# Kernel optimization log

Hardware: AMD Instinct MI355X
Metric: run time of the kernel (lower is better)

Reference implementation:

```python
import jax, jax.numpy as jnp
import numpy as np

B, T, D = 1, 2048, 2048
H, HKV, DH = 32, 8, 64          # head_dim = D // H, n_rep = H // HKV
NREP = H // HKV
WINDOW = 1024
NMETA = 128
EPS = 1e-6
ROPE_BASE = 10000.0


def _rmsnorm(x, w):
    # per-head-dim RMSNorm computed in float32 (matches torch module)
    xf = x.astype(jnp.float32)
    rms = jax.lax.rsqrt(jnp.mean(xf * xf, axis=-1, keepdims=True) + EPS)
    return (w * xf * rms).astype(x.dtype)


def _rope(x, pos):
    # x: [B, h, L, DH], pos: [B, L]; interleaved even/odd rotation
    inv_freq = 1.0 / (ROPE_BASE ** (jnp.arange(0, DH, 2, dtype=jnp.float32) / DH))
    freqs = pos.astype(jnp.float32)[..., None] * inv_freq        # [B, L, DH/2]
    cos = jnp.cos(freqs)[:, None]                                # [B, 1, L, DH/2]
    sin = jnp.sin(freqs)[:, None]
    x1, x2 = x[..., ::2], x[..., 1::2]
    rot = jnp.stack([x1 * cos - x2 * sin, x1 * sin + x2 * cos], axis=-1)
    return rot.reshape(x.shape)


def setup_inputs() -> dict:
    key = jax.random.key(0)
    ks = jax.random.split(key, 5)
    s = 0.02
    return {
        "hidden_states": jax.random.normal(ks[0], (B, T, D), jnp.float32),
        "position_ids": jnp.arange(T, dtype=jnp.int32),
        "Wq": jax.random.normal(ks[1], (H * DH, D), jnp.float32) * s,
        "Wk": jax.random.normal(ks[2], (HKV * DH, D), jnp.float32) * s,
        "Wv": jax.random.normal(ks[3], (HKV * DH, D), jnp.float32) * s,
        "Wo": jax.random.normal(ks[4], (D, H * DH), jnp.float32) * s,
        "q_norm_w": jnp.ones((DH,), jnp.float32),
        "k_norm_w": jnp.ones((DH,), jnp.float32),
    }


def reference(hidden_states, position_ids, Wq, Wk, Wv, Wo, q_norm_w, k_norm_w):
    Bn, Tn, _ = hidden_states.shape
    # projections (nn.Linear: x @ W.T)
    q = (hidden_states @ Wq.T).reshape(Bn, Tn, H, DH).transpose(0, 2, 1, 3)   # [B,H,T,DH]
    k = (hidden_states @ Wk.T).reshape(Bn, Tn, HKV, DH).transpose(0, 2, 1, 3)  # [B,HKV,T,DH]
    v = (hidden_states @ Wv.T).reshape(Bn, Tn, HKV, DH).transpose(0, 2, 1, 3)
    q = _rmsnorm(q, q_norm_w)
    k = _rmsnorm(k, k_norm_w)

    Tk = k.shape[2]  # no kv_cache -> Tk == T
    pos_q = position_ids if position_ids.ndim == 2 else jnp.broadcast_to(position_ids[None], (Bn, Tn))
    pos_k = jnp.broadcast_to(jnp.arange(Tk, dtype=jnp.int32)[None], (Bn, Tk))
    q = _rope(q, pos_q[:, -Tn:])
    k = _rope(k, pos_k)

    # GQA repeat_kv
    k = jnp.broadcast_to(k[:, :, None], (Bn, HKV, NREP, Tk, DH)).reshape(Bn, H, Tk, DH)
    v = jnp.broadcast_to(v[:, :, None], (Bn, HKV, NREP, Tk, DH)).reshape(Bn, H, Tk, DH)

    scores = jnp.einsum('bhqd,bhkd->bhqk', q, k) * (DH ** -0.5)

    # sliding-window + meta-token mask (matches _make_swa_mask)
    q_idx = jnp.arange(Tn)[:, None]
    k_idx = jnp.arange(Tk)[None, :]
    offset = Tk - Tn
    abs_q = q_idx + offset
    win_start = jnp.maximum(abs_q - WINDOW + 1, NMETA)
    allowed = ((k_idx >= win_start) & (k_idx <= abs_q)) | (k_idx < NMETA)
    scores = jnp.where(allowed[None, None], scores, -jnp.inf)

    probs = jax.nn.softmax(scores, axis=-1)
    out = jnp.einsum('bhqk,bhkd->bhqd', probs, v)
    out = out.transpose(0, 2, 1, 3).reshape(Bn, Tn, H * DH)
    return out @ Wo.T
```

## Files before the change

### kernel.cpp

```cpp
#include <hip/hip_runtime.h>
#include <hip/hip_bf16.h>
#include <cstdint>

#define TSEQ 2048
#define DMODEL 2048
#define NHEAD 32
#define NKV 8
#define DHEAD 64
#define QKVN 3072
#define AON 2048

using bf16x8 = __attribute__((ext_vector_type(8))) short;
using bf16x4 = __attribute__((ext_vector_type(4))) short;
using f32x4  = __attribute__((ext_vector_type(4))) float;

__device__ __forceinline__ ushort f2bf(float f) {
  union { float f; uint32_t u; } v; v.f = f;
  uint32_t u = v.u;
  return (ushort)((u + 0x7fffu + ((u >> 16) & 1u)) >> 16);
}

__device__ __forceinline__ float fexp2(float x) {
#if __has_builtin(__builtin_amdgcn_exp2f)
  return __builtin_amdgcn_exp2f(x);
#else
  return __expf(x * 0.69314718055994531f);
#endif
}

__device__ __forceinline__ uint32_t cvtpk(float lo, float hi) {
  uint32_t r;
  asm("v_cvt_pk_bf16_f32 %0, %1, %2" : "=v"(r) : "v"(lo), "v"(hi));
  return r;
}

__device__ __forceinline__ void gload16(const void* g, void* l) {
  __builtin_amdgcn_global_load_lds((const __attribute__((address_space(1))) void*)g,
                                   (__attribute__((address_space(3))) void*)l,
                                   16, 0, 0);
}

#define RG0 1048576
#define RG1 2097152
#define RG2 2359296
#define RG3 2621440
__global__ void k_cvt_all(const float* __restrict__ X, const float* __restrict__ Wq,
                          const float* __restrict__ Wk, const float* __restrict__ Wv,
                          const int* __restrict__ pos,
                          ushort* __restrict__ Xb, ushort* __restrict__ Wqkvb,
                          float4* __restrict__ Tbl) {
  int gid = blockIdx.x * blockDim.x + threadIdx.x;
  if (gid < TSEQ * 32) {
    int t = gid >> 5, jj = gid & 31;
    float invf = fexp2((float)jj * (-0.41524101186092029f));
    float qs, qc, ks, kc;
    __sincosf((float)pos[t] * invf, &qs, &qc);
    __sincosf((float)t * invf, &ks, &kc);
    Tbl[gid] = make_float4(qc * 0.18033688011112043f, qs * 0.18033688011112043f, kc, ks);
  }
  int stride = gridDim.x * blockDim.x;
  for (int i = gid; i < RG3; i += stride) {
    const float4* s; ushort4* d;
    if (i < RG0)      { s = (const float4*)X  + i;         d = (ushort4*)Xb + i; }
    else if (i < RG1) { s = (const float4*)Wq + (i - RG0); d = (ushort4*)Wqkvb + (i - RG0); }
    else if (i < RG2) { s = (const float4*)Wk + (i - RG1); d = (ushort4*)Wqkvb + 1048576 + (i - RG1); }
    else              { s = (const float4*)Wv + (i - RG2); d = (ushort4*)Wqkvb + 1310720 + (i - RG2); }
    float4 v = *s;
    ushort4 o;
    o.x = f2bf(v.x); o.y = f2bf(v.y); o.z = f2bf(v.z); o.w = f2bf(v.w);
    *d = o;
  }
}

__global__ __launch_bounds__(512) void k_gemm_qkv(
    const ushort* __restrict__ A, const ushort* __restrict__ B,
    const float* __restrict__ qw, const float* __restrict__ kw,
    const float4* __restrict__ Tbl,
    ushort* __restrict__ Qb, ushort* __restrict__ Kb, ushort* __restrict__ Vt,
    int M, int N, int K)
{
  __shared__ ushort As[4][128 * 32];
  __shared__ ushort Bs[4][128 * 32];
  const int m0 = blockIdx.y * 128, n0 = blockIdx.x * 128;
  const int tid = threadIdx.x;
  const int w = tid >> 6, lane = tid & 63, lg = lane >> 4, lr = lane & 15;
  const int wr = (w >> 1) * 32, wc = (w & 1) * 64;

  f32x4 acc[2][4];
#pragma unroll
  for (int i = 0; i < 2; ++i)
#pragma unroll
    for (int j = 0; j < 4; ++j) acc[i][j] = (f32x4){0.f, 0.f, 0.f, 0.f};

  const int nt = K >> 5;

  auto stage = [&](int b, int t) {
    const int k0 = t << 5;
    {
      int ci = tid;
      int row = ci >> 2, c = ci & 3;
      int clog = c ^ ((row >> 1) & 3);
      gload16(A + (size_t)(m0 + row) * K + k0 + clog * 8, As[b] + ci * 8);
    }
    {
      int ci = tid;
      int row = ci >> 2, c = ci & 3;
      int clog = c ^ ((row >> 1) & 3);
      gload16(B + (size_t)(n0 + row) * K + k0 + clog * 8, Bs[b] + ci * 8);
    }
  };

  stage(0, 0); stage(1, 1); stage(2, 2);

  for (int t = 0; t < nt; ++t) {
    int rem = nt - t;
    if (rem >= 3)      asm volatile("s_waitcnt vmcnt(4)" ::: "memory");
    else if (rem == 2) asm volatile("s_waitcnt vmcnt(2)" ::: "memory");
    else               asm volatile("s_waitcnt vmcnt(0)" ::: "memory");
    __builtin_amdgcn_s_barrier();
    __builtin_amdgcn_sched_barrier(0);

    const ushort* as = As[t & 3];
    const ushort* bs = Bs[t & 3];
    bf16x8 af[2], bfr[4];
#pragma unroll
    for (int i = 0; i < 2; ++i) {
      int ra = wr + i * 16 + lr;
      af[i] = *reinterpret_cast<const bf16x8*>(as + ra * 32 + ((lg ^ ((ra >> 1) & 3)) << 3));
    }
#pragma unroll
    for (int j = 0; j < 4; ++j) {
      int rb = wc + j * 16 + lr;
      bfr[j] = *reinterpret_cast<const bf16x8*>(bs + rb * 32 + ((lg ^ ((rb >> 1) & 3)) << 3));
    }
    asm volatile("s_waitcnt lgkmcnt(0)" ::: "memory");
    __builtin_amdgcn_sched_barrier(0);

    if (t + 3 < nt) stage((t + 3) & 3, t + 3);

#pragma unroll
    for (int i = 0; i < 2; ++i)
#pragma unroll
      for (int j = 0; j < 4; ++j)
        acc[i][j] = __builtin_amdgcn_mfma_f32_16x16x32_bf16(af[i], bfr[j], acc[i][j], 0, 0, 0);
  }

  const int colunit = (n0 + wc) >> 6;
  if (colunit < 40) {
    const bool isQ = (colunit < 32);
    const float* wn = isQ ? qw : kw;
    float wv[4];
#pragma unroll
    for (int j = 0; j < 4; ++j) wv[j] = wn[j * 16 + lr];
    ushort* dst = isQ ? (Qb + (size_t)colunit * TSEQ * 64)
                      : (Kb + (size_t)(colunit - 32) * TSEQ * 64);
#pragma unroll
    for (int i = 0; i < 2; ++i)
#pragma unroll
      for (int r = 0; r < 4; ++r) {
        int row = m0 + wr + i * 16 + lg * 4 + r;
        float ss = 0.f;
#pragma unroll
        for (int j = 0; j < 4; ++j) { float x = acc[i][j][r]; ss += x * x; }
        ss += __shfl_xor(ss, 1); ss += __shfl_xor(ss, 2);
        ss += __shfl_xor(ss, 4); ss += __shfl_xor(ss, 8);
        float rms = rsqrtf(ss * (1.0f / 64.0f) + 1e-6f);
#pragma unroll
        for (int j = 0; j < 4; ++j) {
          float xh = acc[i][j][r] * rms * wv[j];
          float other = __shfl_xor(xh, 1);
          float4 tb = Tbl[(size_t)row * 32 + j * 8 + (lr >> 1)];
          float c = isQ ? tb.x : tb.z;
          float s = isQ ? tb.y : tb.w;
          float outv = (lr & 1) ? (other * s + xh * c) : (xh * c - other * s);
          dst[(size_t)row * 64 + j * 16 + lr] = f2bf(outv);
        }
      }
  } else {
    const int hv = colunit - 40;
#pragma unroll
    for (int i = 0; i < 2; ++i)
#pragma unroll
      for (int j = 0; j < 4; ++j)
#pragma unroll
        for (int r = 0; r < 4; ++r) {
          int row = m0 + wr + i * 16 + lg * 4 + r;
          Vt[((size_t)hv * 64 + j * 16 + lr) * TSEQ + row] = f2bf(acc[i][j][r]);
        }
  }
}

__global__ __launch_bounds__(256) void k_gemm64(
    const ushort* __restrict__ A, const ushort* __restrict__ B,
    float* __restrict__ C, int M, int N, int K)
{
  __shared__ ushort As[4][64 * 32];
  __shared__ ushort Bs[4][128 * 32];
  const int m0 = blockIdx.y * 64, n0 = blockIdx.x * 128;
  const int tid = threadIdx.x;
  const int w = tid >> 6, lane = tid & 63, lg = lane >> 4, lr = lane & 15;
  const int wr = (w >> 1) * 32, wc = (w & 1) * 64;

  f32x4 acc[2][4];
#pragma unroll
  for (int i = 0; i < 2; ++i)
#pragma unroll
    for (int j = 0; j < 4; ++j) acc[i][j] = (f32x4){0.f, 0.f, 0.f, 0.f};

  const int nt = K >> 5;

  auto stage = [&](int b, int t) {
    const int k0 = t << 5;
    {
      int ci = tid;
      int row = ci >> 2, c = ci & 3;
      int clog = c ^ ((row >> 1) & 3);
      gload16(A + (size_t)(m0 + row) * K + k0 + clog * 8, As[b] + ci * 8);
    }
#pragma unroll
    for (int j = 0; j < 2; ++j) {
      int ci = j * 256 + tid;
      int row = ci >> 2, c = ci & 3;
      int clog = c ^ ((row >> 1) & 3);
      gload16(B + (size_t)(n0 + row) * K + k0 + clog * 8, Bs[b] + ci * 8);
    }
  };

  stage(0, 0); stage(1, 1); stage(2, 2);

  for (int t = 0; t < nt; ++t) {
    int rem = nt - t;
    if (rem >= 3)      asm volatile("s_waitcnt vmcnt(6)" ::: "memory");
    else if (rem == 2) asm volatile("s_waitcnt vmcnt(3)" ::: "memory");
    else               asm volatile("s_waitcnt vmcnt(0)" ::: "memory");
    __builtin_amdgcn_s_barrier();
    __builtin_amdgcn_sched_barrier(0);

    const ushort* as = As[t & 3];
    const ushort* bs = Bs[t & 3];
    bf16x8 af[2], bfr[4];
#pragma unroll
    for (int i = 0; i < 2; ++i) {
      int ra = wr + i * 16 + lr;
      af[i] = *reinterpret_cast<const bf16x8*>(as + ra * 32 + ((lg ^ ((ra >> 1) & 3)) << 3));
    }
#pragma unroll
    for (int j = 0; j < 4; ++j) {
      int rb = wc + j * 16 + lr;
      bfr[j] = *reinterpret_cast<const bf16x8*>(bs + rb * 32 + ((lg ^ ((rb >> 1) & 3)) << 3));
    }
    asm volatile("s_waitcnt lgkmcnt(0)" ::: "memory");
    __builtin_amdgcn_sched_barrier(0);

    if (t + 3 < nt) stage((t + 3) & 3, t + 3);

#pragma unroll
    for (int i = 0; i < 2; ++i)
#pragma unroll
      for (int j = 0; j < 4; ++j)
        acc[i][j] = __builtin_amdgcn_mfma_f32_16x16x32_bf16(af[i], bfr[j], acc[i][j], 0, 0, 0);
  }

#pragma unroll
  for (int i = 0; i < 2; ++i)
#pragma unroll
    for (int j = 0; j < 4; ++j)
#pragma unroll
      for (int r = 0; r < 4; ++r)
        C[(size_t)(m0 + wr + i * 16 + lg * 4 + r) * N + n0 + wc + j * 16 + lr] = acc[i][j][r];
}

__global__ __launch_bounds__(512) void k_attn(
    const ushort* __restrict__ Qb, const ushort* __restrict__ Kb,
    const ushort* __restrict__ Vt, ushort* __restrict__ AO,
    const float* __restrict__ Wo, ushort* __restrict__ Wob)
{
  __shared__ ushort Ks[2][64 * 64];
  __shared__ ushort Vs[2][64 * 64];

  const int h = blockIdx.x;
  const int q0 = ((int)gridDim.y - 1 - (int)blockIdx.y) * 128;
  const int tid = threadIdx.x;
  const int w = tid >> 6, lane = tid & 63;
  const int lg = lane >> 4, lr = lane & 15;
  const int qrow = q0 + w * 16 + lr;

  const ushort* qp = Qb + ((size_t)h * TSEQ + qrow) * 64;
  const bf16x8 qf0 = *reinterpret_cast<const bf16x8*>(qp + lg * 8);
  const bf16x8 qf1 = *reinterpret_cast<const bf16x8*>(qp + 32 + lg * 8);
  const int hk = h >> 2;
  const char* Kh = (const char*)(Kb + (size_t)hk * TSEQ * 64);
  const char* Vh = (const char*)(Vt + (size_t)hk * 64 * TSEQ);

  float m = -1e30f, lsum = 0.0f;
  f32x4 o[4];
#pragma unroll
  for (int dt = 0; dt < 4; ++dt) o[dt] = (f32x4){0.f, 0.f, 0.f, 0.f};

  const int wlo = (q0 >= 1152) ? (q0 - 1024) : 128;
  int nwin = (q0 + 64 - wlo) / 64 + 1;
  if (nwin < 0) nwin = 0;
  const int ntiles = 2 + nwin;
  const int qw0 = q0 + w * 16;
  const int wmaxstart = ((qw0 + 15 - 1023) > 128) ? (qw0 + 15 - 1023) : 128;
  const int wminstart = ((qw0 - 1023) > 128) ? (qw0 - 1023) : 128;
  const int wstart_lane = ((qrow - 1023) > 128) ? (qrow - 1023) : 128;

  auto stage = [&](int b, int kb) {
    int off = tid * 16;
    int r = off >> 7, bp = off & 127;
    int bs = bp ^ ((r & 7) << 4);
    gload16(Kh + (size_t)(kb + r) * 128 + bs, (char*)Ks[b] + off);
    gload16(Vh + (size_t)r * (TSEQ * 2) + (size_t)kb * 2 + bs, (char*)Vs[b] + off);
  };

  stage(0, 0);

  for (int ti = 0; ti < ntiles; ++ti) {
    const int kb = (ti < 2) ? ti * 64 : wlo + (ti - 2) * 64;
    __syncthreads();
    if (ti + 1 < ntiles) {
      const int kb1 = (ti + 1 < 2) ? (ti + 1) * 64 : wlo + (ti - 1) * 64;
      stage((ti + 1) & 1, kb1);
    }
    if (ti >= 2 && ((kb > qw0 + 15) || (kb + 63 < wminstart))) continue;

    const char* ks = (const char*)Ks[ti & 1];
    const char* vs = (const char*)Vs[ti & 1];
    const bool needmask = (ti >= 2) && !((kb + 63 <= qw0) && (kb >= wmaxstart));

    f32x4 st[4];
#pragma unroll
    for (int s = 0; s < 4; ++s) {
      int row = s * 16 + lr;
      int sw = (row & 7) << 4;
      bf16x8 kf0 = *reinterpret_cast<const bf16x8*>(ks + row * 128 + ((lg * 16) ^ sw));
      bf16x8 kf1 = *reinterpret_cast<const bf16x8*>(ks + row * 128 + ((64 + lg * 16) ^ sw));
      f32x4 acc = (f32x4){0.f, 0.f, 0.f, 0.f};
      acc = __builtin_amdgcn_mfma_f32_16x16x32_bf16(kf0, qf0, acc, 0, 0, 0);
      acc = __builtin_amdgcn_mfma_f32_16x16x32_bf16(kf1, qf1, acc, 0, 0, 0);
      st[s] = acc;
    }
    if (needmask) {
#pragma unroll
      for (int s = 0; s < 4; ++s)
#pragma unroll
        for (int r = 0; r < 4; ++r) {
          int key = kb + s * 16 + lg * 4 + r;
          bool ok = (key >= wstart_lane) && (key <= qrow);
          if (!ok) st[s][r] = -1e30f;
        }
    }
    float pmax = st[0][0];
#pragma unroll
    for (int s = 0; s < 4; ++s)
#pragma unroll
      for (int r = 0; r < 4; ++r) pmax = fmaxf(pmax, st[s][r]);
    pmax = fmaxf(pmax, __shfl_xor(pmax, 16));
    pmax = fmaxf(pmax, __shfl_xor(pmax, 32));

    const bool defer = __all(pmax <= m + 8.0f);
    if (!defer) {
      float mnew = fmaxf(m, pmax);
      float sc = fexp2(m - mnew);
      m = mnew;
      lsum *= sc;
#pragma unroll
      for (int dt = 0; dt < 4; ++dt) o[dt] = o[dt] * sc;
    }

    float psum = 0.f;
    bf16x4 pb[4];
#pragma unroll
    for (int s = 0; s < 4; ++s) {
      float e0 = fexp2(st[s][0] - m);
      float e1 = fexp2(st[s][1] - m);
      float e2 = fexp2(st[s][2] - m);
      float e3 = fexp2(st[s][3] - m);
      psum += (e0 + e1) + (e2 + e3);
      union { uint32_t u[2]; bf16x4 b; } pk;
      pk.u[0] = cvtpk(e0, e1);
      pk.u[1] = cvtpk(e2, e3);
      pb[s] = pk.b;
    }
    psum += __shfl_xor(psum, 16);
    psum += __shfl_xor(psum, 32);
    lsum += psum;

#pragma unroll
    for (int dt = 0; dt < 4; ++dt) {
      int row = dt * 16 + lr;
      int sw = (row & 7) << 4;
#pragma unroll
      for (int s = 0; s < 4; ++s) {
        bf16x4 vf = *reinterpret_cast<const bf16x4*>(vs + row * 128 + ((s * 32 + lg * 8) ^ sw));
        o[dt] = __builtin_amdgcn_mfma_f32_16x16x16bf16_1k(vf, pb[s], o[dt], 0, 0, 0);
      }
    }
  }

  float inv = 1.0f / lsum;
#pragma unroll
  for (int dt = 0; dt < 4; ++dt)
#pragma unroll
    for (int r = 0; r < 4; ++r)
      AO[(size_t)qrow * AON + h * 64 + dt * 16 + lg * 4 + r] = f2bf(o[dt][r] * inv);

  {
    int bid = blockIdx.y * gridDim.x + blockIdx.x;
    int idx = bid * 512 + tid;
#pragma unroll
    for (int it = 0; it < 4; ++it) {
      int i = idx + it * 262144;
      float4 v = reinterpret_cast<const float4*>(Wo)[i];
      ushort4 ov;
      ov.x = f2bf(v.x); ov.y = f2bf(v.y); ov.z = f2bf(v.z); ov.w = f2bf(v.w);
      reinterpret_cast<ushort4*>(Wob)[i] = ov;
    }
  }
}

extern "C" void kernel_launch(void* const* d_in, const int* in_sizes, int n_in,
                              void* d_out, int out_size, void* d_ws, size_t ws_size,
                              hipStream_t stream) {
  const float* hs = (const float*)d_in[0];
  const int* pos  = (const int*)d_in[1];
  const float* Wq = (const float*)d_in[2];
  const float* Wk = (const float*)d_in[3];
  const float* Wv = (const float*)d_in[4];
  const float* Wo = (const float*)d_in[5];
  const float* qw = (const float*)d_in[6];
  const float* kw = (const float*)d_in[7];
  float* out = (float*)d_out;

  char* ws = (char*)d_ws;
  ushort* Xb    = (ushort*)ws; ws += (size_t)2048 * 2048 * 2;
  ushort* Wqkvb = (ushort*)ws; ws += (size_t)3072 * 2048 * 2;
  ushort* Wob   = (ushort*)ws; ws += (size_t)2048 * 2048 * 2;
  float4* Tbl   = (float4*)ws; ws += (size_t)2048 * 32 * 16;
  ushort* Qb    = (ushort*)ws; ws += (size_t)32 * 2048 * 64 * 2;
  ushort* Kb    = (ushort*)ws; ws += (size_t)8 * 2048 * 64 * 2;
  ushort* Vt    = (ushort*)ws; ws += (size_t)8 * 64 * 2048 * 2;
  ushort* AO    = (ushort*)ws;

  k_cvt_all<<<2048, 256, 0, stream>>>(hs, Wq, Wk, Wv, pos, Xb, Wqkvb, Tbl);

  k_gemm_qkv<<<dim3(QKVN / 128, TSEQ / 128), 512, 0, stream>>>(
      Xb, Wqkvb, qw, kw, Tbl, Qb, Kb, Vt, TSEQ, QKVN, DMODEL);
  k_attn<<<dim3(NHEAD, TSEQ / 128), 512, 0, stream>>>(Qb, Kb, Vt, AO, Wo, Wob);
  k_gemm64<<<dim3(DMODEL / 128, TSEQ / 64), 256, 0, stream>>>(AO, Wob, out, TSEQ, DMODEL, AON);
}
```

Before: 120.0 us.

## Split-K QKV GEMM with separate RMSNorm/RoPE epilogue kernel

```diff
diff --git a/kernel.cpp b/kernel.cpp
--- a/kernel.cpp
+++ b/kernel.cpp
@@ -20,6 +20,11 @@
   return (ushort)((u + 0x7fffu + ((u >> 16) & 1u)) >> 16);
 }
 
+__device__ __forceinline__ float bf2f(ushort u) {
+  union { uint32_t u; float f; } v; v.u = ((uint32_t)u) << 16;
+  return v.f;
+}
+
 __device__ __forceinline__ float fexp2(float x) {
 #if __has_builtin(__builtin_amdgcn_exp2f)
   return __builtin_amdgcn_exp2f(x);
@@ -46,18 +51,8 @@
 #define RG3 2621440
 __global__ void k_cvt_all(const float* __restrict__ X, const float* __restrict__ Wq,
                           const float* __restrict__ Wk, const float* __restrict__ Wv,
-                          const int* __restrict__ pos,
-                          ushort* __restrict__ Xb, ushort* __restrict__ Wqkvb,
-                          float4* __restrict__ Tbl) {
+                          ushort* __restrict__ Xb, ushort* __restrict__ Wqkvb) {
   int gid = blockIdx.x * blockDim.x + threadIdx.x;
-  if (gid < TSEQ * 32) {
-    int t = gid >> 5, jj = gid & 31;
-    float invf = fexp2((float)jj * (-0.41524101186092029f));
-    float qs, qc, ks, kc;
-    __sincosf((float)pos[t] * invf, &qs, &qc);
-    __sincosf((float)t * invf, &ks, &kc);
-    Tbl[gid] = make_float4(qc * 0.18033688011112043f, qs * 0.18033688011112043f, kc, ks);
-  }
   int stride = gridDim.x * blockDim.x;
   for (int i = gid; i < RG3; i += stride) {
     const float4* s; ushort4* d;
@@ -72,16 +67,16 @@
   }
 }
 
-__global__ __launch_bounds__(512) void k_gemm_qkv(
+__global__ __launch_bounds__(512) void k_gemm_qkv_split(
     const ushort* __restrict__ A, const ushort* __restrict__ B,
-    const float* __restrict__ qw, const float* __restrict__ kw,
-    const float4* __restrict__ Tbl,
-    ushort* __restrict__ Qb, ushort* __restrict__ Kb, ushort* __restrict__ Vt,
+    ushort* __restrict__ P0, ushort* __restrict__ P1,
     int M, int N, int K)
 {
-  __shared__ ushort As[4][128 * 32];
-  __shared__ ushort Bs[4][128 * 32];
+  __shared__ ushort As[3][128 * 32];
+  __shared__ ushort Bs[3][128 * 32];
   const int m0 = blockIdx.y * 128, n0 = blockIdx.x * 128;
+  const int kzbase = blockIdx.z * (K >> 1);
+  ushort* Pz = blockIdx.z ? P1 : P0;
   const int tid = threadIdx.x;
   const int w = tid >> 6, lane = tid & 63, lg = lane >> 4, lr = lane & 15;
   const int wr = (w >> 1) * 32, wc = (w & 1) * 64;
@@ -92,10 +87,10 @@
 #pragma unroll
     for (int j = 0; j < 4; ++j) acc[i][j] = (f32x4){0.f, 0.f, 0.f, 0.f};
 
-  const int nt = K >> 5;
+  const int nt = K >> 6;
 
   auto stage = [&](int b, int t) {
-    const int k0 = t << 5;
+    const int k0 = kzbase + (t << 5);
     {
       int ci = tid;
       int row = ci >> 2, c = ci & 3;
@@ -110,18 +105,17 @@
     }
   };
 
-  stage(0, 0); stage(1, 1); stage(2, 2);
-
+  stage(0, 0); stage(1, 1);
+
+  int b0 = 0;
   for (int t = 0; t < nt; ++t) {
-    int rem = nt - t;
-    if (rem >= 3)      asm volatile("s_waitcnt vmcnt(4)" ::: "memory");
-    else if (rem == 2) asm volatile("s_waitcnt vmcnt(2)" ::: "memory");
-    else               asm volatile("s_waitcnt vmcnt(0)" ::: "memory");
+    if (nt - t >= 2) asm volatile("s_waitcnt vmcnt(2)" ::: "memory");
+    else             asm volatile("s_waitcnt vmcnt(0)" ::: "memory");
     __builtin_amdgcn_s_barrier();
     __builtin_amdgcn_sched_barrier(0);
 
-    const ushort* as = As[t & 3];
-    const ushort* bs = Bs[t & 3];
+    const ushort* as = As[b0];
+    const ushort* bs = Bs[b0];
     bf16x8 af[2], bfr[4];
 #pragma unroll
     for (int i = 0; i < 2; ++i) {
@@ -136,57 +130,66 @@
     asm volatile("s_waitcnt lgkmcnt(0)" ::: "memory");
     __builtin_amdgcn_sched_barrier(0);
 
-    if (t + 3 < nt) stage((t + 3) & 3, t + 3);
+    if (t + 2 < nt) {
+      int b2 = b0 + 2; if (b2 >= 3) b2 -= 3;
+      stage(b2, t + 2);
+    }
 
 #pragma unroll
     for (int i = 0; i < 2; ++i)
 #pragma unroll
       for (int j = 0; j < 4; ++j)
         acc[i][j] = __builtin_amdgcn_mfma_f32_16x16x32_bf16(af[i], bfr[j], acc[i][j], 0, 0, 0);
-  }
-
-  const int colunit = (n0 + wc) >> 6;
-  if (colunit < 40) {
-    const bool isQ = (colunit < 32);
-    const float* wn = isQ ? qw : kw;
-    float wv[4];
-#pragma unroll
-    for (int j = 0; j < 4; ++j) wv[j] = wn[j * 16 + lr];
-    ushort* dst = isQ ? (Qb + (size_t)colunit * TSEQ * 64)
-                      : (Kb + (size_t)(colunit - 32) * TSEQ * 64);
-#pragma unroll
-    for (int i = 0; i < 2; ++i)
+
+    b0 = (b0 + 1 == 3) ? 0 : b0 + 1;
+  }
+
+#pragma unroll
+  for (int i = 0; i < 2; ++i)
+#pragma unroll
+    for (int j = 0; j < 4; ++j)
 #pragma unroll
       for (int r = 0; r < 4; ++r) {
-        int row = m0 + wr + i * 16 + lg * 4 + r;
-        float ss = 0.f;
-#pragma unroll
-        for (int j = 0; j < 4; ++j) { float x = acc[i][j][r]; ss += x * x; }
-        ss += __shfl_xor(ss, 1); ss += __shfl_xor(ss, 2);
-        ss += __shfl_xor(ss, 4); ss += __shfl_xor(ss, 8);
-        float rms = rsqrtf(ss * (1.0f / 64.0f) + 1e-6f);
-#pragma unroll
-        for (int j = 0; j < 4; ++j) {
-          float xh = acc[i][j][r] * rms * wv[j];
-          float other = __shfl_xor(xh, 1);
-          float4 tb = Tbl[(size_t)row * 32 + j * 8 + (lr >> 1)];
-          float c = isQ ? tb.x : tb.z;
-          float s = isQ ? tb.y : tb.w;
-          float outv = (lr & 1) ? (other * s + xh * c) : (xh * c - other * s);
-          dst[(size_t)row * 64 + j * 16 + lr] = f2bf(outv);
-        }
+        size_t idx = (size_t)(m0 + wr + i * 16 + lg * 4 + r) * N + n0 + wc + j * 16 + lr;
+        Pz[idx] = f2bf(acc[i][j][r]);
       }
+}
+
+__global__ __launch_bounds__(256) void k_qkv_epi(
+    const ushort* __restrict__ P0, const ushort* __restrict__ P1,
+    const int* __restrict__ pos,
+    const float* __restrict__ qw, const float* __restrict__ kw,
+    ushort* __restrict__ Qb, ushort* __restrict__ Kb, ushort* __restrict__ Vt)
+{
+  int gw = blockIdx.x * 4 + (threadIdx.x >> 6);
+  int lane = threadIdx.x & 63;
+  int t = gw / 48, u = gw % 48;
+  if (t >= TSEQ) return;
+  if (u < 40) {
+    int col = (u < 32) ? u * 64 + lane : 2048 + (u - 32) * 64 + lane;
+    size_t idx = (size_t)t * QKVN + col;
+    float x = bf2f(P0[idx]) + bf2f(P1[idx]);
+    float ss = x * x;
+#pragma unroll
+    for (int mm = 32; mm; mm >>= 1) ss += __shfl_xor(ss, mm);
+    float r = rsqrtf(ss * (1.0f / 64.0f) + 1e-6f);
+    x = x * r * ((u < 32) ? qw[lane] : kw[lane]);
+    int p = (u < 32) ? pos[t] : t;
+    int j = lane >> 1;
+    float invf = fexp2((float)j * (-0.41524101186092029f));
+    float s, c;
+    __sincosf((float)p * invf, &s, &c);
+    float other = __shfl_xor(x, 1);
+    float out = (lane & 1) ? (other * s + x * c) : (x * c - other * s);
+    if (u < 32)
+      Qb[((size_t)u * TSEQ + t) * 64 + lane] = f2bf(out * 0.18033688011112043f);
+    else
+      Kb[((size_t)(u - 32) * TSEQ + t) * 64 + lane] = f2bf(out);
   } else {
-    const int hv = colunit - 40;
-#pragma unroll
-    for (int i = 0; i < 2; ++i)
-#pragma unroll
-      for (int j = 0; j < 4; ++j)
-#pragma unroll
-        for (int r = 0; r < 4; ++r) {
-          int row = m0 + wr + i * 16 + lg * 4 + r;
-          Vt[((size_t)hv * 64 + j * 16 + lr) * TSEQ + row] = f2bf(acc[i][j][r]);
-        }
+    int hv = u - 40;
+    size_t idx = (size_t)t * QKVN + 2560 + hv * 64 + lane;
+    float x = bf2f(P0[idx]) + bf2f(P1[idx]);
+    Vt[((size_t)hv * 64 + lane) * TSEQ + t] = f2bf(x);
   }
 }
 
@@ -436,17 +439,20 @@
   char* ws = (char*)d_ws;
   ushort* Xb    = (ushort*)ws; ws += (size_t)2048 * 2048 * 2;
   ushort* Wqkvb = (ushort*)ws; ws += (size_t)3072 * 2048 * 2;
-  ushort* Wob   = (ushort*)ws; ws += (size_t)2048 * 2048 * 2;
-  float4* Tbl   = (float4*)ws; ws += (size_t)2048 * 32 * 16;
   ushort* Qb    = (ushort*)ws; ws += (size_t)32 * 2048 * 64 * 2;
   ushort* Kb    = (ushort*)ws; ws += (size_t)8 * 2048 * 64 * 2;
   ushort* Vt    = (ushort*)ws; ws += (size_t)8 * 64 * 2048 * 2;
-  ushort* AO    = (ushort*)ws;
-
-  k_cvt_all<<<2048, 256, 0, stream>>>(hs, Wq, Wk, Wv, pos, Xb, Wqkvb, Tbl);
-
-  k_gemm_qkv<<<dim3(QKVN / 128, TSEQ / 128), 512, 0, stream>>>(
-      Xb, Wqkvb, qw, kw, Tbl, Qb, Kb, Vt, TSEQ, QKVN, DMODEL);
+  char* region = ws;
+  ushort* P0  = (ushort*)region;
+  ushort* P1  = (ushort*)(region + (size_t)2048 * 3072 * 2);
+  ushort* Wob = (ushort*)region;
+  ushort* AO  = (ushort*)(region + (size_t)2048 * 2048 * 2);
+
+  k_cvt_all<<<2048, 256, 0, stream>>>(hs, Wq, Wk, Wv, Xb, Wqkvb);
+
+  k_gemm_qkv_split<<<dim3(QKVN / 128, TSEQ / 128, 2), 512, 0, stream>>>(
+      Xb, Wqkvb, P0, P1, TSEQ, QKVN, DMODEL);
+  k_qkv_epi<<<(TSEQ * 48) / 4, 256, 0, stream>>>(P0, P1, pos, qw, kw, Qb, Kb, Vt);
   k_attn<<<dim3(NHEAD, TSEQ / 128), 512, 0, stream>>>(Qb, Kb, Vt, AO, Wo, Wob);
   k_gemm64<<<dim3(DMODEL / 128, TSEQ / 64), 256, 0, stream>>>(AO, Wob, out, TSEQ, DMODEL, AON);
 }
```

Result: slower. 135.5 us (+12.9%).
